# Performance work log

Measured on AMD Instinct MI355X. Metric: run time of the kernel, lower is better.

The kernel has to match this reference:

```python
import jax, jax.numpy as jnp
import numpy as np

N_NODES = 50000
N_EDGES = 800000
NODE_DIM = 128
EDGE_DIM = 64
HIDDEN = 256


def setup_inputs() -> dict:
    key = jax.random.key(0)
    ks = jax.random.split(key, 12)
    glorot = lambda k, fi, fo: jax.random.normal(k, (fi, fo), jnp.float32) * (2.0 / (fi + fo)) ** 0.5
    return {
        "node_features": jax.random.normal(ks[0], (N_NODES, NODE_DIM), jnp.float32),
        "edge_features": jax.random.normal(ks[1], (N_EDGES, EDGE_DIM), jnp.float32),
        "src": jax.random.randint(ks[2], (N_EDGES,), 0, N_NODES),
        "dst": jax.random.randint(ks[3], (N_EDGES,), 0, N_NODES),
        # edge_update MLP: (2*node_dim + edge_dim) -> hidden -> edge_dim
        "We1": glorot(ks[4], 2 * NODE_DIM + EDGE_DIM, HIDDEN),
        "be1": jnp.zeros((HIDDEN,), jnp.float32),
        "We2": glorot(ks[5], HIDDEN, EDGE_DIM),
        "be2": jnp.zeros((EDGE_DIM,), jnp.float32),
        # node_update MLP: (node_dim + edge_dim) -> hidden -> node_dim
        "Wn1": glorot(ks[6], NODE_DIM + EDGE_DIM, HIDDEN),
        "bn1": jnp.zeros((HIDDEN,), jnp.float32),
        "Wn2": glorot(ks[7], HIDDEN, NODE_DIM),
        "bn2": jnp.zeros((NODE_DIM,), jnp.float32),
    }


def reference(node_features, edge_features, src, dst, We1, be1, We2, be2, Wn1, bn1, Wn2, bn2):
    # message: per-edge MLP on [src_h, e, dst_h]
    concat = jnp.concatenate(
        [node_features[src], edge_features, node_features[dst]], axis=1
    )  # [E, 2*node_dim + edge_dim]
    e_upd = jax.nn.relu(concat @ We1 + be1) @ We2 + be2  # [E, edge_dim]

    # reduce: sum incoming messages per destination node
    e_sum = jax.ops.segment_sum(e_upd, dst, num_segments=node_features.shape[0])  # [N, edge_dim]
    node_in = jnp.concatenate([node_features, e_sum], axis=1)  # [N, node_dim + edge_dim]
    h_new = jax.nn.relu(node_in @ Wn1 + bn1) @ Wn2 + bn2  # [N, node_dim]

    # DGL only applies reduce_func to nodes with at least one incoming edge
    deg = jax.ops.segment_sum(jnp.ones_like(dst, jnp.float32), dst, num_segments=node_features.shape[0])
    h_out = jnp.where(deg[:, None] > 0, h_new, node_features)

    # original module never writes e_updated back: returned edge features are the inputs
    return h_out, edge_features
```

## Files before the change

### kernel.cpp

```cpp
#include <hip/hip_runtime.h>

#define N_NODES 50000
#define N_EDGES 800000
#define NODE_DIM 128
#define EDGE_DIM 64
#define HIDDEN 256
#define K_N 192

typedef __attribute__((ext_vector_type(8))) short bf16x8;
typedef __attribute__((ext_vector_type(4))) float f32x4;
typedef __attribute__((ext_vector_type(16))) float f32x16;
typedef unsigned short u16;
typedef unsigned int u32;

#define MFMA16 __builtin_amdgcn_mfma_f32_16x16x32_bf16
#define MFMA32 __builtin_amdgcn_mfma_f32_32x32x16_bf16

__device__ inline u16 f2bf(float f) {
  u32 u = __builtin_bit_cast(u32, f);
  u += 0x7fffu + ((u >> 16) & 1u);
  return (u16)(u >> 16);
}
__device__ inline float bf2f(u16 u) {
  u32 x = ((u32)u) << 16;
  return __builtin_bit_cast(float, x);
}
__device__ inline u32 pack2(float a, float b) {
  return (u32)f2bf(a) | ((u32)f2bf(b) << 16);
}
__device__ inline void st_bf4(u16* p, float4 v) {
  ushort4 r;
  r.x = f2bf(v.x); r.y = f2bf(v.y); r.z = f2bf(v.z); r.w = f2bf(v.w);
  *reinterpret_cast<ushort4*>(p) = r;
}

__global__ void prep_weights(const float* __restrict__ We1, const float* __restrict__ We2,
                             const float* __restrict__ Wn1, const float* __restrict__ Wn2,
                             const float* __restrict__ be2, const int* __restrict__ dst,
                             u16* __restrict__ w1st, u16* __restrict__ w1dt,
                             u16* __restrict__ w1ef, u16* __restrict__ w2y,
                             u16* __restrict__ wn1t, u16* __restrict__ wn2t,
                             float* __restrict__ b2p, int* __restrict__ hist) {
  const int stride = gridDim.x * blockDim.x;
  const int tid = blockIdx.x * blockDim.x + threadIdx.x;
  for (int i = tid; i < HIDDEN * NODE_DIM; i += stride) {
    int h = i >> 7, k = i & 127;
    w1st[i] = f2bf(We1[k * HIDDEN + h]);
    w1dt[i] = f2bf(We1[(192 + k) * HIDDEN + h]);
  }
  for (int i = tid; i < 8 * 4 * 64 * 8; i += stride) {
    int jj = i & 7;
    int l = (i >> 3) & 63;
    int kb = (i >> 9) & 3;
    int ht = i >> 11;
    int h = ht * 32 + (l & 31);
    int kloc = kb * 16 + (l >> 5) * 8 + jj;
    w1ef[i] = f2bf(We1[(128 + kloc) * HIDDEN + h]);
  }
  for (int i = tid; i < EDGE_DIM * HIDDEN; i += stride) {
    int jj = i & 7;
    int l = (i >> 3) & 63;
    int t2 = (i >> 9) & 1;
    int kb2 = i >> 10;
    int out = t2 * 32 + (l & 31);
    int hi = l >> 5;
    int k = kb2 * 16 + (jj & 3) + 8 * (jj >> 2) + 4 * hi;
    w2y[i] = f2bf(We2[k * EDGE_DIM + out]);
  }
  for (int i = tid; i < HIDDEN * K_N; i += stride) {
    int n = i / K_N, k = i % K_N;
    wn1t[i] = f2bf(Wn1[k * HIDDEN + n]);
  }
  for (int i = tid; i < NODE_DIM * HIDDEN; i += stride) {
    int n = i / HIDDEN, k = i % HIDDEN;
    wn2t[i] = f2bf(Wn2[k * NODE_DIM + n]);
  }
  for (int i = tid; i < EDGE_DIM; i += stride) {
    int t2 = i >> 5, hi = (i >> 4) & 1, r = i & 15;
    b2p[i] = be2[t2 * 32 + (r & 3) + 8 * (r >> 2) + 4 * hi];
  }
  for (int i = tid; i < N_EDGES; i += stride)
    atomicAdd(&hist[dst[i]], 1);
}

#define NB_P 782
#define SA_P 136
#define SH   264

__global__ __launch_bounds__(256) void pgemm_kernel(
    const float* __restrict__ nf, const u16* __restrict__ w1st,
    const u16* __restrict__ w1dt, const float* __restrict__ be1,
    u16* __restrict__ P_src, u16* __restrict__ P_dst)
{
  const int table = (blockIdx.x >= NB_P) ? 1 : 0;
  const int b = blockIdx.x - table * NB_P;
  const u16* w = table ? w1dt : w1st;
  u16* P = table ? P_dst : P_src;

  __shared__ u16 A[64 * SH];
  const int tid = threadIdx.x;
  const int n0 = b * 64;
  const float4* nf4 = reinterpret_cast<const float4*>(nf);

  #pragma unroll
  for (int p = 0; p < 8; ++p) {
    int i = p * 256 + tid;
    int row = i >> 5, c4 = i & 31;
    int rg = min(n0 + row, N_NODES - 1);
    float4 v = nf4[(size_t)rg * 32 + c4];
    st_bf4(&A[row * SA_P + c4 * 4], v);
  }
  __syncthreads();

  const int wave = tid >> 6, lane = tid & 63;
  const int lr = lane & 15;
  const int lk = (lane >> 4) * 8;

  f32x4 acc[4][4] = {};
  #pragma unroll
  for (int kb = 0; kb < 4; ++kb) {
    const int ko = kb * 32 + lk;
    bf16x8 a[4], bb[4];
    #pragma unroll
    for (int mt = 0; mt < 4; ++mt)
      a[mt] = *reinterpret_cast<const bf16x8*>(&A[(mt * 16 + lr) * SA_P + ko]);
    #pragma unroll
    for (int nt = 0; nt < 4; ++nt)
      bb[nt] = *reinterpret_cast<const bf16x8*>(&w[(size_t)(wave * 64 + nt * 16 + lr) * 128 + ko]);
    #pragma unroll
    for (int mt = 0; mt < 4; ++mt)
      #pragma unroll
      for (int nt = 0; nt < 4; ++nt)
        acc[mt][nt] = MFMA16(a[mt], bb[nt], acc[mt][nt], 0, 0, 0);
  }
  __syncthreads();

  u16* H = A;
  #pragma unroll
  for (int mt = 0; mt < 4; ++mt)
    #pragma unroll
    for (int nt = 0; nt < 4; ++nt) {
      int col = wave * 64 + nt * 16 + lr;
      float bias = table ? 0.f : be1[col];
      #pragma unroll
      for (int j = 0; j < 4; ++j) {
        int row = mt * 16 + (lane >> 4) * 4 + j;
        H[row * SH + col] = f2bf(acc[mt][nt][j] + bias);
      }
    }
  __syncthreads();

  #pragma unroll
  for (int p = 0; p < 16; ++p) {
    int u = p * 256 + tid;
    int row = u >> 6, cg = u & 63;
    int hi = cg >> 5, ht = (cg >> 2) & 7, q = cg & 3;
    int hbase = ht * 32 + 8 * q + 4 * hi;
    int n = n0 + row;
    if (n < N_NODES) {
      ushort4 v = *reinterpret_cast<const ushort4*>(&H[row * SH + hbase]);
      *reinterpret_cast<ushort4*>(&P[(size_t)n * 256 + cg * 4]) = v;
    }
  }
}

#define NB_SCAN 196

__global__ void scanA_kernel(const int* __restrict__ hist, int* __restrict__ eid) {
  __shared__ int red[256];
  int gid = blockIdx.x * 256 + threadIdx.x;
  int v = (gid < N_NODES) ? hist[gid] : 0;
  red[threadIdx.x] = v;
  __syncthreads();
  for (int d = 128; d > 0; d >>= 1) {
    if (threadIdx.x < d) red[threadIdx.x] += red[threadIdx.x + d];
    __syncthreads();
  }
  if (threadIdx.x == 0) eid[blockIdx.x] = red[0];
}

__global__ void scanB_kernel(int* __restrict__ eid, int* __restrict__ off) {
  __shared__ int ssum[256];
  int tid = threadIdx.x;
  int v = (tid < NB_SCAN) ? eid[tid] : 0;
  ssum[tid] = v;
  __syncthreads();
  for (int d = 1; d < 256; d <<= 1) {
    int t = (tid >= d) ? ssum[tid - d] : 0;
    __syncthreads();
    ssum[tid] += t;
    __syncthreads();
  }
  if (tid < NB_SCAN) eid[256 + tid] = ssum[tid] - v;
  if (tid == 255) off[N_NODES] = ssum[255];
}

__global__ void scanC_kernel(const int* __restrict__ hist, const int* __restrict__ eid,
                             int* __restrict__ off, int* __restrict__ cursor,
                             float* __restrict__ e_sum) {
  __shared__ int ssum[256];
  int tid = threadIdx.x;
  int gid = blockIdx.x * 256 + tid;
  int base = eid[256 + blockIdx.x];
  int v = (gid < N_NODES) ? hist[gid] : 0;
  ssum[tid] = v;
  __syncthreads();
  for (int d = 1; d < 256; d <<= 1) {
    int t = (tid >= d) ? ssum[tid - d] : 0;
    __syncthreads();
    ssum[tid] += t;
    __syncthreads();
  }
  if (gid < N_NODES) {
    int o = base + ssum[tid] - v;
    off[gid] = o;
    cursor[gid] = o;
    float4 z = {0.f, 0.f, 0.f, 0.f};
    float4* ez = reinterpret_cast<float4*>(e_sum + (size_t)gid * 64);
    #pragma unroll
    for (int q = 0; q < 16; ++q) ez[q] = z;
  }
}

__global__ void scatter_kernel(const int* __restrict__ src, const int* __restrict__ dst,
                               int* __restrict__ cursor, int* __restrict__ eid,
                               int* __restrict__ csr_src, int* __restrict__ csr_dst) {
  int e = blockIdx.x * blockDim.x + threadIdx.x;
  if (e < N_EDGES) {
    int d = dst[e];
    int pos = atomicAdd(&cursor[d], 1);
    eid[pos] = e;
    csr_src[pos] = src[e];
    csr_dst[pos] = d;
  }
}

__global__ __launch_bounds__(256, 4) void edge_mlp(
    const u16* __restrict__ P_src, const u16* __restrict__ P_dst,
    const float* __restrict__ ef,
    const int* __restrict__ eid, const int* __restrict__ csr_src,
    const int* __restrict__ csr_dst,
    const u16* __restrict__ w1ef, const u16* __restrict__ w2y,
    const float* __restrict__ b2p,
    float* __restrict__ e_sum, float* __restrict__ out_edge)
{
  __shared__ char shmem[33280];
  u16* W1e = reinterpret_cast<u16*>(shmem);
  float* bounce = reinterpret_cast<float*>(shmem);

  const int tid = threadIdx.x;
  const int wv = tid >> 6, lane = tid & 63;
  const int ecol = lane & 31;
  const int hi = lane >> 5;
  const int e0 = blockIdx.x * 128;
  const int pos = e0 + wv * 32 + ecol;

  {
    const uint4* s = reinterpret_cast<const uint4*>(w1ef);
    uint4* d = reinterpret_cast<uint4*>(W1e);
    #pragma unroll
    for (int j = 0; j < 8; ++j) d[j * 256 + tid] = s[j * 256 + tid];
  }

  {
    const float4* ef4 = reinterpret_cast<const float4*>(ef);
    float4* oe4 = reinterpret_cast<float4*>(out_edge);
    #pragma unroll
    for (int p = 0; p < 8; ++p) {
      size_t i = (size_t)e0 * 16 + p * 256 + tid;
      oe4[i] = ef4[i];
    }
  }

  const int e    = eid[pos];
  const int srcn = csr_src[pos];
  const int dstn = csr_dst[pos];

  bf16x8 efr[4];
  #pragma unroll
  for (int kb = 0; kb < 4; ++kb) {
    const float* ep = ef + (size_t)e * 64 + kb * 16 + hi * 8;
    float4 lo = *reinterpret_cast<const float4*>(ep);
    float4 hv = *reinterpret_cast<const float4*>(ep + 4);
    bf16x8 v;
    v[0] = (short)f2bf(lo.x); v[1] = (short)f2bf(lo.y);
    v[2] = (short)f2bf(lo.z); v[3] = (short)f2bf(lo.w);
    v[4] = (short)f2bf(hv.x); v[5] = (short)f2bf(hv.y);
    v[6] = (short)f2bf(hv.z); v[7] = (short)f2bf(hv.w);
    efr[kb] = v;
  }

  __syncthreads();

  f32x16 acc2[2];
  #pragma unroll
  for (int t2 = 0; t2 < 2; ++t2) {
    const float* bp = b2p + t2 * 32 + hi * 16;
    #pragma unroll
    for (int r = 0; r < 16; ++r) acc2[t2][r] = bp[r];
  }

  const u16* psb = P_src + (size_t)srcn * 256 + hi * 128;
  const u16* pdb = P_dst + (size_t)dstn * 256 + hi * 128;

  #pragma unroll
  for (int ht = 0; ht < 8; ++ht) {
    bf16x8 a0 = *reinterpret_cast<const bf16x8*>(psb + ht * 16);
    bf16x8 a1 = *reinterpret_cast<const bf16x8*>(psb + ht * 16 + 8);
    bf16x8 d0 = *reinterpret_cast<const bf16x8*>(pdb + ht * 16);
    bf16x8 d1 = *reinterpret_cast<const bf16x8*>(pdb + ht * 16 + 8);
    f32x16 acc;
    #pragma unroll
    for (int r = 0; r < 8; ++r) {
      acc[r]     = bf2f((u16)a0[r]) + bf2f((u16)d0[r]);
      acc[8 + r] = bf2f((u16)a1[r]) + bf2f((u16)d1[r]);
    }

    #pragma unroll
    for (int kb = 0; kb < 4; ++kb) {
      bf16x8 wf = *reinterpret_cast<const bf16x8*>(W1e + ((ht * 4 + kb) * 64 + lane) * 8);
      acc = MFMA32(wf, efr[kb], acc, 0, 0, 0);
    }

    #pragma unroll
    for (int s2 = 0; s2 < 2; ++s2) {
      bf16x8 hf;
      u32* hw = reinterpret_cast<u32*>(&hf);
      #pragma unroll
      for (int m = 0; m < 4; ++m)
        hw[m] = pack2(fmaxf(acc[s2 * 8 + 2 * m], 0.f),
                      fmaxf(acc[s2 * 8 + 2 * m + 1], 0.f));
      #pragma unroll
      for (int t2 = 0; t2 < 2; ++t2) {
        bf16x8 wf2 = *reinterpret_cast<const bf16x8*>(
            w2y + ((size_t)((ht * 2 + s2) * 2 + t2) * 64 + lane) * 8);
        acc2[t2] = MFMA32(wf2, hf, acc2[t2], 0, 0, 0);
      }
    }
  }

  __syncthreads();

  {
    const int lp = wv * 32 + ecol;
    #pragma unroll
    for (int t2 = 0; t2 < 2; ++t2)
      #pragma unroll
      for (int r = 0; r < 16; ++r) {
        int o = t2 * 32 + (r & 3) + 8 * (r >> 2) + 4 * hi;
        bounce[lp * 65 + o] = acc2[t2][r];
      }
  }

  {
    const int d = lane;
    const int base = wv * 32;
    float s = bounce[base * 65 + d];
    int cur = __shfl(dstn, 0, 64);
    #pragma unroll 4
    for (int i = 1; i < 32; ++i) {
      int nx = __shfl(dstn, i, 64);
      float v = bounce[(base + i) * 65 + d];
      if (nx == cur) {
        s += v;
      } else {
        atomicAdd(&e_sum[(size_t)cur * 64 + d], s);
        cur = nx;
        s = v;
      }
    }
    atomicAdd(&e_sum[(size_t)cur * 64 + d], s);
  }
}

#define SA_N 200

__global__ __launch_bounds__(256) void node_kernel(
    const float* __restrict__ nf, const float* __restrict__ e_sum,
    const int* __restrict__ hist,
    const u16* __restrict__ w1, const float* __restrict__ b1,
    const u16* __restrict__ w2, const float* __restrict__ b2,
    float* __restrict__ hout)
{
  __shared__ u16 A[64 * SH];
  const int tid = threadIdx.x;
  const int n0 = blockIdx.x * 64;

  const float4* nf4 = reinterpret_cast<const float4*>(nf);
  const float4* es4 = reinterpret_cast<const float4*>(e_sum);

  #pragma unroll
  for (int p = 0; p < 8; ++p) {
    int i = p * 256 + tid;
    int row = i >> 5, c4 = i & 31;
    int rg = min(n0 + row, N_NODES - 1);
    float4 v = nf4[(size_t)rg * 32 + c4];
    st_bf4(&A[row * SA_N + c4 * 4], v);
  }
  #pragma unroll
  for (int p = 0; p < 4; ++p) {
    int i = p * 256 + tid;
    int row = i >> 4, c4 = i & 15;
    int rg = min(n0 + row, N_NODES - 1);
    float4 v = es4[(size_t)rg * 16 + c4];
    st_bf4(&A[row * SA_N + 128 + c4 * 4], v);
  }
  __syncthreads();

  const int wave = tid >> 6, lane = tid & 63;
  const int lr = lane & 15;
  const int lk = (lane >> 4) * 8;

  f32x4 acc[4][4] = {};
  for (int kb = 0; kb < K_N / 32; ++kb) {
    const int ko = kb * 32 + lk;
    bf16x8 a[4], b[4];
    #pragma unroll
    for (int mt = 0; mt < 4; ++mt)
      a[mt] = *reinterpret_cast<const bf16x8*>(&A[(mt * 16 + lr) * SA_N + ko]);
    #pragma unroll
    for (int nt = 0; nt < 4; ++nt)
      b[nt] = *reinterpret_cast<const bf16x8*>(&w1[(size_t)(wave * 64 + nt * 16 + lr) * K_N + ko]);
    #pragma unroll
    for (int mt = 0; mt < 4; ++mt)
      #pragma unroll
      for (int nt = 0; nt < 4; ++nt)
        acc[mt][nt] = MFMA16(a[mt], b[nt], acc[mt][nt], 0, 0, 0);
  }
  __syncthreads();

  u16* H = A;
  #pragma unroll
  for (int mt = 0; mt < 4; ++mt)
    #pragma unroll
    for (int nt = 0; nt < 4; ++nt) {
      int col = wave * 64 + nt * 16 + lr;
      float bias = b1[col];
      #pragma unroll
      for (int j = 0; j < 4; ++j) {
        int row = mt * 16 + (lane >> 4) * 4 + j;
        float h = acc[mt][nt][j] + bias;
        H[row * SH + col] = f2bf(h > 0.f ? h : 0.f);
      }
    }
  __syncthreads();

  f32x4 acc2[8] = {};
  for (int kb = 0; kb < HIDDEN / 32; ++kb) {
    const int ko = kb * 32 + lk;
    bf16x8 a = *reinterpret_cast<const bf16x8*>(&H[(wave * 16 + lr) * SH + ko]);
    #pragma unroll
    for (int nt = 0; nt < 8; ++nt) {
      bf16x8 b = *reinterpret_cast<const bf16x8*>(&w2[(size_t)(nt * 16 + lr) * HIDDEN + ko]);
      acc2[nt] = MFMA16(a, b, acc2[nt], 0, 0, 0);
    }
  }
  #pragma unroll
  for (int nt = 0; nt < 8; ++nt) {
    int col = nt * 16 + lr;
    float bias = b2[col];
    #pragma unroll
    for (int j = 0; j < 4; ++j) {
      int row = wave * 16 + (lane >> 4) * 4 + j;
      int rg = n0 + row;
      if (rg < N_NODES) {
        float v = acc2[nt][j] + bias;
        hout[(size_t)rg * NODE_DIM + col] =
            (hist[rg] != 0) ? v : nf[(size_t)rg * NODE_DIM + col];
      }
    }
  }
}

extern "C" void kernel_launch(void* const* d_in, const int* in_sizes, int n_in,
                              void* d_out, int out_size, void* d_ws, size_t ws_size,
                              hipStream_t stream) {
  const float* nf  = (const float*)d_in[0];
  const float* ef  = (const float*)d_in[1];
  const int*   src = (const int*)d_in[2];
  const int*   dst = (const int*)d_in[3];
  const float* We1 = (const float*)d_in[4];
  const float* be1 = (const float*)d_in[5];
  const float* We2 = (const float*)d_in[6];
  const float* be2 = (const float*)d_in[7];
  const float* Wn1 = (const float*)d_in[8];
  const float* bn1 = (const float*)d_in[9];
  const float* Wn2 = (const float*)d_in[10];
  const float* bn2 = (const float*)d_in[11];

  float* hout = (float*)d_out;
  float* out_edge = hout + (size_t)N_NODES * NODE_DIM;

  char* ws = (char*)d_ws;
  int*   hist    = (int*)ws;
  int*   off     = (int*)(ws + 200000);
  int*   cursor  = (int*)(ws + 400016);
  int*   eid     = (int*)(ws + 600016);
  int*   csr_src = (int*)(ws + 3800016);
  int*   csr_dst = (int*)(ws + 7000016);
  float* e_sum   = (float*)(ws + 10200016);
  u16*   w1ef    = (u16*)(ws + 23000016);
  u16*   w1st    = (u16*)(ws + 23032784);
  u16*   w1dt    = (u16*)(ws + 23098320);
  u16*   w2y     = (u16*)(ws + 23163856);
  u16*   wn1t    = (u16*)(ws + 23196624);
  u16*   wn2t    = (u16*)(ws + 23294928);
  float* b2p     = (float*)(ws + 23360464);
  u16*   P_src   = (u16*)(ws + 23360720);
  u16*   P_dst   = (u16*)(ws + 48960720);

  hipMemsetAsync(hist, 0, 200000, stream);
  prep_weights<<<512, 256, 0, stream>>>(We1, We2, Wn1, Wn2, be2, dst,
                                        w1st, w1dt, w1ef, w2y, wn1t, wn2t,
                                        b2p, hist);
  pgemm_kernel<<<2 * NB_P, 256, 0, stream>>>(nf, w1st, w1dt, be1, P_src, P_dst);
  scanA_kernel<<<NB_SCAN, 256, 0, stream>>>(hist, eid);
  scanB_kernel<<<1, 256, 0, stream>>>(eid, off);
  scanC_kernel<<<NB_SCAN, 256, 0, stream>>>(hist, eid, off, cursor, e_sum);
  scatter_kernel<<<(N_EDGES + 255) / 256, 256, 0, stream>>>(src, dst, cursor, eid,
                                                            csr_src, csr_dst);

  edge_mlp<<<N_EDGES / 128, 256, 0, stream>>>(P_src, P_dst, ef, eid, csr_src,
                                              csr_dst, w1ef, w2y, b2p,
                                              e_sum, out_edge);
  node_kernel<<<(N_NODES + 63) / 64, 256, 0, stream>>>(nf, e_sum, hist,
                                                       wn1t, bn1, wn2t, bn2, hout);
}
```

Before: 524.2 us.

## Pre-sort bf16 edge features in scatter, prefetch P rows, fuse pgemm tables

When the workspace is large enough, the scatter kernel writes edge features converted to bf16 in CSR order, so edge_mlp reads them contiguously instead of gathering fp32 rows through eid. The P_src/P_dst loads in edge_mlp are software-pipelined one ht step ahead. pgemm now computes both tables in one block to reuse the staged node tile, and bf16 packing uses the v_cvt_pk_bf16_f32 instruction. The trade-off is an extra 102MB workspace write and read, plus higher register pressure in edge_mlp from the prefetch.

```diff
diff --git a/kernel.cpp b/kernel.cpp
--- a/kernel.cpp
+++ b/kernel.cpp
@@ -25,8 +25,10 @@
   u32 x = ((u32)u) << 16;
   return __builtin_bit_cast(float, x);
 }
-__device__ inline u32 pack2(float a, float b) {
-  return (u32)f2bf(a) | ((u32)f2bf(b) << 16);
+__device__ inline u32 cvt_pk(float a, float b) {
+  u32 r;
+  asm("v_cvt_pk_bf16_f32 %0, %1, %2" : "=v"(r) : "v"(a), "v"(b));
+  return r;
 }
 __device__ inline void st_bf4(u16* p, float4 v) {
   ushort4 r;
@@ -92,14 +94,10 @@
     const u16* __restrict__ w1dt, const float* __restrict__ be1,
     u16* __restrict__ P_src, u16* __restrict__ P_dst)
 {
-  const int table = (blockIdx.x >= NB_P) ? 1 : 0;
-  const int b = blockIdx.x - table * NB_P;
-  const u16* w = table ? w1dt : w1st;
-  u16* P = table ? P_dst : P_src;
-
-  __shared__ u16 A[64 * SH];
+  __shared__ u16 A[64 * SA_P];
+  __shared__ u16 H[64 * SH];
   const int tid = threadIdx.x;
-  const int n0 = b * 64;
+  const int n0 = blockIdx.x * 64;
   const float4* nf4 = reinterpret_cast<const float4*>(nf);
 
   #pragma unroll
@@ -116,50 +114,54 @@
   const int lr = lane & 15;
   const int lk = (lane >> 4) * 8;
 
-  f32x4 acc[4][4] = {};
-  #pragma unroll
-  for (int kb = 0; kb < 4; ++kb) {
-    const int ko = kb * 32 + lk;
-    bf16x8 a[4], bb[4];
+  for (int table = 0; table < 2; ++table) {
+    const u16* w = table ? w1dt : w1st;
+    u16* P = table ? P_dst : P_src;
+
+    f32x4 acc[4][4] = {};
+    #pragma unroll
+    for (int kb = 0; kb < 4; ++kb) {
+      const int ko = kb * 32 + lk;
+      bf16x8 a[4], bb[4];
+      #pragma unroll
+      for (int mt = 0; mt < 4; ++mt)
+        a[mt] = *reinterpret_cast<const bf16x8*>(&A[(mt * 16 + lr) * SA_P + ko]);
+      #pragma unroll
+      for (int nt = 0; nt < 4; ++nt)
+        bb[nt] = *reinterpret_cast<const bf16x8*>(&w[(size_t)(wave * 64 + nt * 16 + lr) * 128 + ko]);
+      #pragma unroll
+      for (int mt = 0; mt < 4; ++mt)
+        #pragma unroll
+        for (int nt = 0; nt < 4; ++nt)
+          acc[mt][nt] = MFMA16(a[mt], bb[nt], acc[mt][nt], 0, 0, 0);
+    }
+    __syncthreads();
+
     #pragma unroll
     for (int mt = 0; mt < 4; ++mt)
-      a[mt] = *reinterpret_cast<const bf16x8*>(&A[(mt * 16 + lr) * SA_P + ko]);
-    #pragma unroll
-    for (int nt = 0; nt < 4; ++nt)
-      bb[nt] = *reinterpret_cast<const bf16x8*>(&w[(size_t)(wave * 64 + nt * 16 + lr) * 128 + ko]);
-    #pragma unroll
-    for (int mt = 0; mt < 4; ++mt)
-      #pragma unroll
-      for (int nt = 0; nt < 4; ++nt)
-        acc[mt][nt] = MFMA16(a[mt], bb[nt], acc[mt][nt], 0, 0, 0);
-  }
-  __syncthreads();
-
-  u16* H = A;
-  #pragma unroll
-  for (int mt = 0; mt < 4; ++mt)
-    #pragma unroll
-    for (int nt = 0; nt < 4; ++nt) {
-      int col = wave * 64 + nt * 16 + lr;
-      float bias = table ? 0.f : be1[col];
-      #pragma unroll
-      for (int j = 0; j < 4; ++j) {
-        int row = mt * 16 + (lane >> 4) * 4 + j;
-        H[row * SH + col] = f2bf(acc[mt][nt][j] + bias);
-      }
-    }
-  __syncthreads();
-
-  #pragma unroll
-  for (int p = 0; p < 16; ++p) {
-    int u = p * 256 + tid;
-    int row = u >> 6, cg = u & 63;
-    int hi = cg >> 5, ht = (cg >> 2) & 7, q = cg & 3;
-    int hbase = ht * 32 + 8 * q + 4 * hi;
-    int n = n0 + row;
-    if (n < N_NODES) {
-      ushort4 v = *reinterpret_cast<const ushort4*>(&H[row * SH + hbase]);
-      *reinterpret_cast<ushort4*>(&P[(size_t)n * 256 + cg * 4]) = v;
+      #pragma unroll
+      for (int nt = 0; nt < 4; ++nt) {
+        int col = wave * 64 + nt * 16 + lr;
+        float bias = table ? 0.f : be1[col];
+        #pragma unroll
+        for (int j = 0; j < 4; ++j) {
+          int row = mt * 16 + (lane >> 4) * 4 + j;
+          H[row * SH + col] = f2bf(acc[mt][nt][j] + bias);
+        }
+      }
+    __syncthreads();
+
+    #pragma unroll
+    for (int p = 0; p < 16; ++p) {
+      int u = p * 256 + tid;
+      int row = u >> 6, cg = u & 63;
+      int hi = cg >> 5, ht = (cg >> 2) & 7, q = cg & 3;
+      int hbase = ht * 32 + 8 * q + 4 * hi;
+      int n = n0 + row;
+      if (n < N_NODES) {
+        ushort4 v = *reinterpret_cast<const ushort4*>(&H[row * SH + hbase]);
+        *reinterpret_cast<ushort4*>(&P[(size_t)n * 256 + cg * 4]) = v;
+      }
     }
   }
 }
@@ -222,22 +224,38 @@
   }
 }
 
+template<bool EFB>
 __global__ void scatter_kernel(const int* __restrict__ src, const int* __restrict__ dst,
+                               const float* __restrict__ ef,
                                int* __restrict__ cursor, int* __restrict__ eid,
-                               int* __restrict__ csr_src, int* __restrict__ csr_dst) {
+                               int* __restrict__ csr_src, int* __restrict__ csr_dst,
+                               u16* __restrict__ csr_efb) {
   int e = blockIdx.x * blockDim.x + threadIdx.x;
   if (e < N_EDGES) {
     int d = dst[e];
     int pos = atomicAdd(&cursor[d], 1);
-    eid[pos] = e;
     csr_src[pos] = src[e];
     csr_dst[pos] = d;
-  }
-}
-
+    if (EFB) {
+      const float4* s = reinterpret_cast<const float4*>(ef + (size_t)e * 64);
+      #pragma unroll
+      for (int q = 0; q < 16; q += 2) {
+        float4 v0 = s[q], v1 = s[q + 1];
+        uint4 r;
+        r.x = cvt_pk(v0.x, v0.y); r.y = cvt_pk(v0.z, v0.w);
+        r.z = cvt_pk(v1.x, v1.y); r.w = cvt_pk(v1.z, v1.w);
+        *reinterpret_cast<uint4*>(csr_efb + (size_t)pos * 64 + q * 4) = r;
+      }
+    } else {
+      eid[pos] = e;
+    }
+  }
+}
+
+template<bool EFB>
 __global__ __launch_bounds__(256, 4) void edge_mlp(
     const u16* __restrict__ P_src, const u16* __restrict__ P_dst,
-    const float* __restrict__ ef,
+    const float* __restrict__ ef, const u16* __restrict__ csr_efb,
     const int* __restrict__ eid, const int* __restrict__ csr_src,
     const int* __restrict__ csr_dst,
     const u16* __restrict__ w1ef, const u16* __restrict__ w2y,
@@ -272,22 +290,27 @@
     }
   }
 
-  const int e    = eid[pos];
   const int srcn = csr_src[pos];
   const int dstn = csr_dst[pos];
 
   bf16x8 efr[4];
-  #pragma unroll
-  for (int kb = 0; kb < 4; ++kb) {
-    const float* ep = ef + (size_t)e * 64 + kb * 16 + hi * 8;
-    float4 lo = *reinterpret_cast<const float4*>(ep);
-    float4 hv = *reinterpret_cast<const float4*>(ep + 4);
-    bf16x8 v;
-    v[0] = (short)f2bf(lo.x); v[1] = (short)f2bf(lo.y);
-    v[2] = (short)f2bf(lo.z); v[3] = (short)f2bf(lo.w);
-    v[4] = (short)f2bf(hv.x); v[5] = (short)f2bf(hv.y);
-    v[6] = (short)f2bf(hv.z); v[7] = (short)f2bf(hv.w);
-    efr[kb] = v;
+  if (EFB) {
+    const u16* eb = csr_efb + (size_t)pos * 64 + hi * 8;
+    #pragma unroll
+    for (int kb = 0; kb < 4; ++kb)
+      efr[kb] = *reinterpret_cast<const bf16x8*>(eb + kb * 16);
+  } else {
+    const int e = eid[pos];
+    #pragma unroll
+    for (int kb = 0; kb < 4; ++kb) {
+      const float* ep = ef + (size_t)e * 64 + kb * 16 + hi * 8;
+      float4 lo = *reinterpret_cast<const float4*>(ep);
+      float4 hv = *reinterpret_cast<const float4*>(ep + 4);
+      u32 w[4];
+      w[0] = cvt_pk(lo.x, lo.y); w[1] = cvt_pk(lo.z, lo.w);
+      w[2] = cvt_pk(hv.x, hv.y); w[3] = cvt_pk(hv.z, hv.w);
+      efr[kb] = __builtin_bit_cast(bf16x8, *reinterpret_cast<uint4*>(w));
+    }
   }
 
   __syncthreads();
@@ -303,17 +326,26 @@
   const u16* psb = P_src + (size_t)srcn * 256 + hi * 128;
   const u16* pdb = P_dst + (size_t)dstn * 256 + hi * 128;
 
+  bf16x8 pa0 = *reinterpret_cast<const bf16x8*>(psb);
+  bf16x8 pa1 = *reinterpret_cast<const bf16x8*>(psb + 8);
+  bf16x8 pd0 = *reinterpret_cast<const bf16x8*>(pdb);
+  bf16x8 pd1 = *reinterpret_cast<const bf16x8*>(pdb + 8);
+
   #pragma unroll
   for (int ht = 0; ht < 8; ++ht) {
-    bf16x8 a0 = *reinterpret_cast<const bf16x8*>(psb + ht * 16);
-    bf16x8 a1 = *reinterpret_cast<const bf16x8*>(psb + ht * 16 + 8);
-    bf16x8 d0 = *reinterpret_cast<const bf16x8*>(pdb + ht * 16);
-    bf16x8 d1 = *reinterpret_cast<const bf16x8*>(pdb + ht * 16 + 8);
+    bf16x8 na0, na1, nd0, nd1;
+    if (ht < 7) {
+      na0 = *reinterpret_cast<const bf16x8*>(psb + (ht + 1) * 16);
+      na1 = *reinterpret_cast<const bf16x8*>(psb + (ht + 1) * 16 + 8);
+      nd0 = *reinterpret_cast<const bf16x8*>(pdb + (ht + 1) * 16);
+      nd1 = *reinterpret_cast<const bf16x8*>(pdb + (ht + 1) * 16 + 8);
+    }
+
     f32x16 acc;
     #pragma unroll
     for (int r = 0; r < 8; ++r) {
-      acc[r]     = bf2f((u16)a0[r]) + bf2f((u16)d0[r]);
-      acc[8 + r] = bf2f((u16)a1[r]) + bf2f((u16)d1[r]);
+      acc[r]     = bf2f((u16)pa0[r]) + bf2f((u16)pd0[r]);
+      acc[8 + r] = bf2f((u16)pa1[r]) + bf2f((u16)pd1[r]);
     }
 
     #pragma unroll
@@ -328,8 +360,8 @@
       u32* hw = reinterpret_cast<u32*>(&hf);
       #pragma unroll
       for (int m = 0; m < 4; ++m)
-        hw[m] = pack2(fmaxf(acc[s2 * 8 + 2 * m], 0.f),
-                      fmaxf(acc[s2 * 8 + 2 * m + 1], 0.f));
+        hw[m] = cvt_pk(fmaxf(acc[s2 * 8 + 2 * m], 0.f),
+                       fmaxf(acc[s2 * 8 + 2 * m + 1], 0.f));
       #pragma unroll
       for (int t2 = 0; t2 < 2; ++t2) {
         bf16x8 wf2 = *reinterpret_cast<const bf16x8*>(
@@ -337,6 +369,8 @@
         acc2[t2] = MFMA32(wf2, hf, acc2[t2], 0, 0, 0);
       }
     }
+
+    pa0 = na0; pa1 = na1; pd0 = nd0; pd1 = nd1;
   }
 
   __syncthreads();
@@ -508,21 +542,31 @@
   float* b2p     = (float*)(ws + 23360464);
   u16*   P_src   = (u16*)(ws + 23360720);
   u16*   P_dst   = (u16*)(ws + 48960720);
+  u16*   csr_efb = (u16*)(ws + 74560720);
+  const size_t NEED_EFB = 176960720;
+  const int efb = (ws_size >= NEED_EFB) ? 1 : 0;
 
   hipMemsetAsync(hist, 0, 200000, stream);
   prep_weights<<<512, 256, 0, stream>>>(We1, We2, Wn1, Wn2, be2, dst,
                                         w1st, w1dt, w1ef, w2y, wn1t, wn2t,
                                         b2p, hist);
-  pgemm_kernel<<<2 * NB_P, 256, 0, stream>>>(nf, w1st, w1dt, be1, P_src, P_dst);
+  pgemm_kernel<<<NB_P, 256, 0, stream>>>(nf, w1st, w1dt, be1, P_src, P_dst);
   scanA_kernel<<<NB_SCAN, 256, 0, stream>>>(hist, eid);
   scanB_kernel<<<1, 256, 0, stream>>>(eid, off);
   scanC_kernel<<<NB_SCAN, 256, 0, stream>>>(hist, eid, off, cursor, e_sum);
-  scatter_kernel<<<(N_EDGES + 255) / 256, 256, 0, stream>>>(src, dst, cursor, eid,
-                                                            csr_src, csr_dst);
-
-  edge_mlp<<<N_EDGES / 128, 256, 0, stream>>>(P_src, P_dst, ef, eid, csr_src,
-                                              csr_dst, w1ef, w2y, b2p,
-                                              e_sum, out_edge);
+  if (efb) {
+    scatter_kernel<true><<<(N_EDGES + 255) / 256, 256, 0, stream>>>(
+        src, dst, ef, cursor, eid, csr_src, csr_dst, csr_efb);
+    edge_mlp<true><<<N_EDGES / 128, 256, 0, stream>>>(
+        P_src, P_dst, ef, csr_efb, eid, csr_src, csr_dst,
+        w1ef, w2y, b2p, e_sum, out_edge);
+  } else {
+    scatter_kernel<false><<<(N_EDGES + 255) / 256, 256, 0, stream>>>(
+        src, dst, ef, cursor, eid, csr_src, csr_dst, csr_efb);
+    edge_mlp<false><<<N_EDGES / 128, 256, 0, stream>>>(
+        P_src, P_dst, ef, csr_efb, eid, csr_src, csr_dst,
+        w1ef, w2y, b2p, e_sum, out_edge);
+  }
   node_kernel<<<(N_NODES + 63) / 64, 256, 0, stream>>>(nf, e_sum, hist,
                                                        wn1t, bn1, wn2t, bn2, hout);
 }
```

Measured after the change: 553.7 us. 1.06x slower.
